# Kernel optimization log

Hardware: AMD Instinct MI355X
Metric: run time of the kernel (lower is better)

## Reference

```python
import jax, jax.numpy as jnp
import numpy as np

H = 64  # hidden_dimension
F = 8   # number_of_input_features
P = 64  # prediction_length
B = 1024
T = 512


def _lstm_cell(x, h, c, Wih, Whh, bih, bhh):
    # PyTorch gate order: input, forget, cell(g), output
    gates = x @ Wih.T + h @ Whh.T + (bih + bhh)  # [B, 4H]
    i, f, g, o = jnp.split(gates, 4, axis=-1)
    c_new = jax.nn.sigmoid(f) * c + jax.nn.sigmoid(i) * jnp.tanh(g)
    h_new = jax.nn.sigmoid(o) * jnp.tanh(c_new)
    return h_new, c_new


def setup_inputs() -> dict:
    key = jax.random.key(0)
    ks = jax.random.split(key, 11)
    s = 1.0 / np.sqrt(H)
    u = lambda k, shape: jax.random.uniform(k, shape, jnp.float32, -s, s)
    return {
        "input_sequence": jax.random.normal(ks[0], (B, T, F), jnp.float32),
        "enc_Wih": u(ks[1], (4 * H, F)),
        "enc_Whh": u(ks[2], (4 * H, H)),
        "enc_bih": u(ks[3], (4 * H,)),
        "enc_bhh": u(ks[4], (4 * H,)),
        "dec_Wih": u(ks[5], (4 * H, F)),
        "dec_Whh": u(ks[6], (4 * H, H)),
        "dec_bih": u(ks[7], (4 * H,)),
        "dec_bhh": u(ks[8], (4 * H,)),
        "fc_W": u(ks[9], (F, H)),
        "fc_b": u(ks[10], (F,)),
    }


def reference(input_sequence, enc_Wih, enc_Whh, enc_bih, enc_bhh,
              dec_Wih, dec_Whh, dec_bih, dec_bhh, fc_W, fc_b):
    Bn = input_sequence.shape[0]
    h0 = jnp.zeros((Bn, H), input_sequence.dtype)
    c0 = jnp.zeros((Bn, H), input_sequence.dtype)

    # ---- Encoder: scan over time ----
    xs = jnp.swapaxes(input_sequence, 0, 1)  # [T, B, F]

    def enc_step(carry, x_t):
        h, c = carry
        h, c = _lstm_cell(x_t, h, c, enc_Wih, enc_Whh, enc_bih, enc_bhh)
        return (h, c), None

    (h, c), _ = jax.lax.scan(enc_step, (h0, c0), xs)

    x_last = input_sequence[:, -1, :]  # [B, F]

    def dec_step(carry, _):
        h, c, x = carry
        h, c = _lstm_cell(x, h, c, dec_Wih, dec_Whh, dec_bih, dec_bhh)
        pred = h @ fc_W.T + fc_b  # [B, F]
        return (h, c, pred), pred

    _, preds = jax.lax.scan(dec_step, (h, c, x_last), None, length=P)
    return jnp.swapaxes(preds, 0, 1)  # [B, P, F]
```

## Files before the change

### kernel.cpp

```cpp
#include <hip/hip_runtime.h>


#define Hh 64
#define Ff 8
#define Tt 512
#define Pp 64
#define BATCH 1024
#define MB 4
#define NBLK (BATCH / MB)
#define ROWS 72
#define ABUF (16 * ROWS + 64)
#define XSTRIDE 32

typedef __attribute__((ext_vector_type(8))) _Float16 half8;
typedef __attribute__((ext_vector_type(4))) _Float16 half4;
typedef __attribute__((ext_vector_type(4))) float f32x4;

#define LOG2E  1.44269504088896340736f
#define K2LOG2 2.88538008177792681472f

#define MFMA16(a, b, c) __builtin_amdgcn_mfma_f32_16x16x32_f16(a, b, c, 0, 0, 0)

__device__ __forceinline__ float rcp_(float x)  { return __builtin_amdgcn_rcpf(x); }
__device__ __forceinline__ float exp2_(float x) { return __builtin_amdgcn_exp2f(x); }
__device__ __forceinline__ int arow_base(int m) { return m * ROWS + (m & 3) * 16; }

__device__ __forceinline__ void load_wfrags(
    const float* __restrict__ Whh, const float* __restrict__ Wih,
    int wv, int q, int col, half8 w0[4], half8 w1[4], half8 wx[4])
{
    #pragma unroll
    for (int Tg = 0; Tg < 4; ++Tg) {
        int g = Tg * 64 + wv * 16 + col;
        float sc = (Tg == 2) ? K2LOG2 : LOG2E;
        const float* r0 = Whh + g * 64 + q * 8;
        #pragma unroll
        for (int j = 0; j < 8; ++j) {
            w0[Tg][j] = (_Float16)(r0[j] * sc);
            w1[Tg][j] = (_Float16)(r0[32 + j] * sc);
            wx[Tg][j] = (q == 0) ? (_Float16)(Wih[g * 8 + j] * sc) : (_Float16)0.f;
        }
    }
}

__device__ __forceinline__ void pchain(half8 ax, const half8 wx[4],
                                       const f32x4 biasv[4], f32x4 P[4])
{
    P[2] = MFMA16(ax, wx[2], biasv[2]);
    P[0] = MFMA16(ax, wx[0], biasv[0]);
    P[1] = MFMA16(ax, wx[1], biasv[1]);
    P[3] = MFMA16(ax, wx[3], biasv[3]);
}

__device__ __forceinline__ void qgates(half8 a0, half8 a1,
    const half8 w0[4], const half8 w1[4], const f32x4 P[4], f32x4 Q[4])
{
    Q[2] = MFMA16(a0, w0[2], P[2]);
    Q[2] = MFMA16(a1, w1[2], Q[2]);
    Q[0] = MFMA16(a0, w0[0], P[0]);
    Q[0] = MFMA16(a1, w1[0], Q[0]);
    Q[1] = MFMA16(a0, w0[1], P[1]);
    Q[1] = MFMA16(a1, w1[1], Q[1]);
    Q[3] = MFMA16(a0, w0[3], P[3]);
    Q[3] = MFMA16(a1, w1[3], Q[3]);
}

__device__ __forceinline__ float cellf(const f32x4 Q[4], float& cS)
{
    float eg = exp2_(Q[2][0]);
    float ei = exp2_(-Q[0][0]);
    float it = (eg - 1.f) * rcp_((1.f + ei) * (1.f + eg));
    float ef = exp2_(-Q[1][0]);
    float sf = rcp_(1.f + ef);
    float eo = exp2_(-Q[3][0]);
    float so   = rcp_(1.f + eo);
    float m2so = -2.f * so;
    cS = __builtin_fmaf(sf, cS, K2LOG2 * it);
    float cc = __builtin_amdgcn_fmed3f(cS, -60.f, 60.f);
    float ec = exp2_(cc);
    float rc = rcp_(1.f + ec);
    return __builtin_fmaf(m2so, rc, so);
}

__global__ __launch_bounds__(256, 1)
void seq2seq_v16(const float* __restrict__ x_seq,
                 const float* __restrict__ eWih, const float* __restrict__ eWhh,
                 const float* __restrict__ ebih, const float* __restrict__ ebhh,
                 const float* __restrict__ dWih, const float* __restrict__ dWhh,
                 const float* __restrict__ dbih, const float* __restrict__ dbhh,
                 const float* __restrict__ fcW,  const float* __restrict__ fcb,
                 float* __restrict__ out)
{
    __shared__ __align__(16) _Float16 xs[(Tt + 2) * XSTRIDE];
    __shared__ __align__(16) _Float16 A0[ABUF];
    __shared__ __align__(16) _Float16 A1[ABUF];

    const int tid  = threadIdx.x;
    const int wv   = tid >> 6;
    const int lane = tid & 63;
    const int q    = lane >> 4;
    const int col  = lane & 15;
    const int u    = wv * 16 + col;
    const int b0   = blockIdx.x * MB;

    half8 w0[4], w1[4], wx[4];
    load_wfrags(eWhh, eWih, wv, q, col, w0, w1, wx);
    f32x4 biasv[4];
    #pragma unroll
    for (int Tg = 0; Tg < 4; ++Tg) {
        int g = Tg * 64 + u;
        float sc = (Tg == 2) ? K2LOG2 : LOG2E;
        float bv = (ebih[g] + ebhh[g]) * sc;
        biasv[Tg] = (f32x4){bv, bv, bv, bv};
    }

    { int* Z0 = (int*)A0; int* Z1 = (int*)A1;
      for (int i = tid; i < ABUF / 2; i += 256) { Z0[i] = 0; Z1[i] = 0; } }
    if (tid < 32) ((int*)xs)[Tt * 16 + tid] = 0;
    for (int i = tid; i < MB * Tt * 2; i += 256) {
        int b   = i >> 10;
        int rem = i & 1023;
        int t   = rem >> 1;
        int f4  = (rem & 1) * 4;
        const float* src = x_seq + ((size_t)(b0 + b) * Tt + t) * Ff + f4;
        half4 s = { (_Float16)src[0], (_Float16)src[1], (_Float16)src[2], (_Float16)src[3] };
        *(half4*)(&xs[t * XSTRIDE + b * 8 + f4]) = s;
    }
    __syncthreads();

    const _Float16* arA = A0 + arow_base(col) + q * 8;
    const _Float16* arB = A1 + arow_base(col) + q * 8;
    _Float16* hwA = A0 + 4 * q * ROWS + u;
    _Float16* hwB = A1 + 4 * q * ROWS + u;
    const _Float16* xq = xs + (col >> 2) * 8;

    float cS = 0.f;
    f32x4 P[4];
    {   half8 ax = *(const half8*)(xq);
        pchain(ax, wx, biasv, P);
        xq += XSTRIDE; }

    for (int t = 0; t < Tt; t += 2) {
        __syncthreads();
        {
            half8 a0 = *(const half8*)(arA);
            half8 a1 = *(const half8*)(arA + 32);
            half8 ax = *(const half8*)(xq); xq += XSTRIDE;
            f32x4 Q[4];
            qgates(a0, a1, w0, w1, P, Q);
            pchain(ax, wx, biasv, P);
            float hn = cellf(Q, cS);
            *hwB = (_Float16)hn;
        }
        __syncthreads();
        {
            half8 a0 = *(const half8*)(arB);
            half8 a1 = *(const half8*)(arB + 32);
            half8 ax = *(const half8*)(xq); xq += XSTRIDE;
            f32x4 Q[4];
            qgates(a0, a1, w0, w1, P, Q);
            pchain(ax, wx, biasv, P);
            float hn = cellf(Q, cS);
            *hwA = (_Float16)hn;
        }
    }

    half8 axl = *(const half8*)(xs + (Tt - 1) * XSTRIDE + (col >> 2) * 8);

    half8 wp0[4], wp1[4];
    f32x4 biasp[4];
    #pragma unroll
    for (int Tg = 0; Tg < 4; ++Tg) {
        int g = Tg * 64 + u;
        float sc = (Tg == 2) ? K2LOG2 : LOG2E;
        #pragma unroll
        for (int j = 0; j < 8; ++j) {
            int k0 = q * 8 + j;
            float v0 = dWhh[g * 64 + k0];
            float v1 = dWhh[g * 64 + 32 + k0];
            w0[Tg][j] = (_Float16)(v0 * sc);
            w1[Tg][j] = (_Float16)(v1 * sc);
            wx[Tg][j] = (q == 0) ? (_Float16)(dWih[g * 8 + j] * sc) : (_Float16)0.f;
            float s0 = v0, s1 = v1;
            #pragma unroll
            for (int f = 0; f < 8; ++f) {
                float wif = dWih[g * 8 + f];
                s0 = __builtin_fmaf(wif, fcW[f * 64 + k0], s0);
                s1 = __builtin_fmaf(wif, fcW[f * 64 + 32 + k0], s1);
            }
            wp0[Tg][j] = (_Float16)(s0 * sc);
            wp1[Tg][j] = (_Float16)(s1 * sc);
        }
        float bb = dbih[g] + dbhh[g];
        float bp = bb;
        #pragma unroll
        for (int f = 0; f < 8; ++f) bp = __builtin_fmaf(dWih[g * 8 + f], fcb[f], bp);
        biasv[Tg] = (f32x4){bb * sc, bb * sc, bb * sc, bb * sc};
        biasp[Tg] = (f32x4){bp * sc, bp * sc, bp * sc, bp * sc};
    }
    half8 wf0, wf1;
    f32x4 biasf;
    {
        #pragma unroll
        for (int j = 0; j < 8; ++j) {
            wf0[j] = (col < 8) ? (_Float16)fcW[col * 64 + q * 8 + j]      : (_Float16)0.f;
            wf1[j] = (col < 8) ? (_Float16)fcW[col * 64 + 32 + q * 8 + j] : (_Float16)0.f;
        }
        float fb = (col < 8) ? fcb[col] : 0.f;
        biasf = (f32x4){fb, fb, fb, fb};
    }

    float* predbuf = (float*)xs;
    const bool pw = (wv == 0) && (col < 8);

    pchain(axl, wx, biasv, P);
    __syncthreads();
    {
        half8 a0 = *(const half8*)(arA);
        half8 a1 = *(const half8*)(arA + 32);
        f32x4 Q[4];
        qgates(a0, a1, w0, w1, P, Q);
        float hn = cellf(Q, cS);
        *hwB = (_Float16)hn;
    }

    for (int p = 1; p < Pp; ++p) {
        __syncthreads();
        const _Float16* ar = (p & 1) ? arB : arA;
        _Float16*       hw = (p & 1) ? hwA : hwB;
        half8 a0 = *(const half8*)(ar);
        half8 a1 = *(const half8*)(ar + 32);
        f32x4 Q[4];
        qgates(a0, a1, wp0, wp1, biasp, Q);
        f32x4 F = MFMA16(a0, wf0, biasf);
        F       = MFMA16(a1, wf1, F);
        float hn = cellf(Q, cS);
        *hw = (_Float16)hn;
        if (pw) predbuf[q * (Pp * Ff) + (p - 1) * Ff + col] = F[0];
    }

    __syncthreads();
    {
        half8 a0 = *(const half8*)(arA);
        half8 a1 = *(const half8*)(arA + 32);
        f32x4 F = MFMA16(a0, wf0, biasf);
        F       = MFMA16(a1, wf1, F);
        if (pw) predbuf[q * (Pp * Ff) + (Pp - 1) * Ff + col] = F[0];
    }
    __syncthreads();

    {
        f32x4* out4 = (f32x4*)out + (size_t)b0 * (Pp * Ff / 4);
        const f32x4* pb4 = (const f32x4*)predbuf;
        for (int i = tid; i < MB * Pp * Ff / 4; i += 256)
            out4[i] = pb4[i];
    }
}

extern "C" void kernel_launch(void* const* d_in, const int* in_sizes, int n_in,
                              void* d_out, int out_size, void* d_ws, size_t ws_size,
                              hipStream_t stream) {
    (void)in_sizes; (void)n_in; (void)d_ws; (void)ws_size; (void)out_size;
    hipLaunchKernelGGL(seq2seq_v16, dim3(NBLK), dim3(256), 0, stream,
                       (const float*)d_in[0],
                       (const float*)d_in[1], (const float*)d_in[2],
                       (const float*)d_in[3], (const float*)d_in[4],
                       (const float*)d_in[5], (const float*)d_in[6],
                       (const float*)d_in[7], (const float*)d_in[8],
                       (const float*)d_in[9], (const float*)d_in[10],
                       (float*)d_out);
}
```

Before: 218.4 us.

## Compute input projection with one MFMA per step via lane-selected operand

```diff
diff --git a/kernel.cpp b/kernel.cpp
--- a/kernel.cpp
+++ b/kernel.cpp
@@ -26,8 +26,8 @@
 __device__ __forceinline__ int arow_base(int m) { return m * ROWS + (m & 3) * 16; }
 
 __device__ __forceinline__ void load_wfrags(
-    const float* __restrict__ Whh, const float* __restrict__ Wih,
-    int wv, int q, int col, half8 w0[4], half8 w1[4], half8 wx[4])
+    const float* __restrict__ Whh, int wv, int q, int col,
+    half8 w0[4], half8 w1[4])
 {
     #pragma unroll
     for (int Tg = 0; Tg < 4; ++Tg) {
@@ -38,31 +38,38 @@
         for (int j = 0; j < 8; ++j) {
             w0[Tg][j] = (_Float16)(r0[j] * sc);
             w1[Tg][j] = (_Float16)(r0[32 + j] * sc);
-            wx[Tg][j] = (q == 0) ? (_Float16)(Wih[g * 8 + j] * sc) : (_Float16)0.f;
-        }
-    }
-}
-
-__device__ __forceinline__ void pchain(half8 ax, const half8 wx[4],
-                                       const f32x4 biasv[4], f32x4 P[4])
-{
-    P[2] = MFMA16(ax, wx[2], biasv[2]);
-    P[0] = MFMA16(ax, wx[0], biasv[0]);
-    P[1] = MFMA16(ax, wx[1], biasv[1]);
-    P[3] = MFMA16(ax, wx[3], biasv[3]);
+        }
+    }
 }
 
 __device__ __forceinline__ void qgates(half8 a0, half8 a1,
-    const half8 w0[4], const half8 w1[4], const f32x4 P[4], f32x4 Q[4])
-{
-    Q[2] = MFMA16(a0, w0[2], P[2]);
+    const half8 w0[4], const half8 w1[4], const f32x4 Ci[4], f32x4 Q[4])
+{
+    Q[2] = MFMA16(a0, w0[2], Ci[2]);
     Q[2] = MFMA16(a1, w1[2], Q[2]);
-    Q[0] = MFMA16(a0, w0[0], P[0]);
+    Q[0] = MFMA16(a0, w0[0], Ci[0]);
     Q[0] = MFMA16(a1, w1[0], Q[0]);
-    Q[1] = MFMA16(a0, w0[1], P[1]);
+    Q[1] = MFMA16(a0, w0[1], Ci[1]);
     Q[1] = MFMA16(a1, w1[1], Q[1]);
-    Q[3] = MFMA16(a0, w0[3], P[3]);
+    Q[3] = MFMA16(a0, w0[3], Ci[3]);
     Q[3] = MFMA16(a1, w1[3], Q[3]);
+}
+
+__device__ __forceinline__ float cellf3(const f32x4 Q[4], f32x4 P4, float& cS)
+{
+    float eg = exp2_(Q[2][0] + P4[2]);
+    float ei = exp2_(-(Q[0][0] + P4[0]));
+    float it = (eg - 1.f) * rcp_((1.f + ei) * (1.f + eg));
+    float ef = exp2_(-(Q[1][0] + P4[1]));
+    float sf = rcp_(1.f + ef);
+    float eo = exp2_(-(Q[3][0] + P4[3]));
+    float so   = rcp_(1.f + eo);
+    float m2so = -2.f * so;
+    cS = __builtin_fmaf(sf, cS, K2LOG2 * it);
+    float cc = __builtin_amdgcn_fmed3f(cS, -60.f, 60.f);
+    float ec = exp2_(cc);
+    float rc = rcp_(1.f + ec);
+    return __builtin_fmaf(m2so, rc, so);
 }
 
 __device__ __forceinline__ float cellf(const f32x4 Q[4], float& cS)
@@ -83,7 +90,7 @@
 }
 
 __global__ __launch_bounds__(256, 1)
-void seq2seq_v16(const float* __restrict__ x_seq,
+void seq2seq_v18(const float* __restrict__ x_seq,
                  const float* __restrict__ eWih, const float* __restrict__ eWhh,
                  const float* __restrict__ ebih, const float* __restrict__ ebhh,
                  const float* __restrict__ dWih, const float* __restrict__ dWhh,
@@ -102,9 +109,12 @@
     const int col  = lane & 15;
     const int u    = wv * 16 + col;
     const int b0   = blockIdx.x * MB;
-
-    half8 w0[4], w1[4], wx[4];
-    load_wfrags(eWhh, eWih, wv, q, col, w0, w1, wx);
+    const bool selq = (q == (col & 3));
+    const half8 hz = {};
+    const f32x4 Zv = {0.f, 0.f, 0.f, 0.f};
+
+    half8 w0[4], w1[4];
+    load_wfrags(eWhh, wv, q, col, w0, w1);
     f32x4 biasv[4];
     #pragma unroll
     for (int Tg = 0; Tg < 4; ++Tg) {
@@ -113,6 +123,10 @@
         float bv = (ebih[g] + ebhh[g]) * sc;
         biasv[Tg] = (f32x4){bv, bv, bv, bv};
     }
+    half8 Bx;
+    #pragma unroll
+    for (int j = 0; j < 8; ++j)
+        Bx[j] = (_Float16)(eWih[(q * 64 + u) * 8 + j] * ((q == 2) ? K2LOG2 : LOG2E));
 
     { int* Z0 = (int*)A0; int* Z1 = (int*)A1;
       for (int i = tid; i < ABUF / 2; i += 256) { Z0[i] = 0; Z1[i] = 0; } }
@@ -135,32 +149,33 @@
     const _Float16* xq = xs + (col >> 2) * 8;
 
     float cS = 0.f;
-    f32x4 P[4];
-    {   half8 ax = *(const half8*)(xq);
-        pchain(ax, wx, biasv, P);
-        xq += XSTRIDE; }
+    f32x4 P4a, P4b;
+    half8 xvA, xvB;
+    {   half8 xv0 = *(const half8*)(xq); xq += XSTRIDE;
+        xvA        = *(const half8*)(xq); xq += XSTRIDE;
+        P4a = MFMA16(selq ? xv0 : hz, Bx, Zv); }
 
     for (int t = 0; t < Tt; t += 2) {
         __syncthreads();
         {
             half8 a0 = *(const half8*)(arA);
             half8 a1 = *(const half8*)(arA + 32);
-            half8 ax = *(const half8*)(xq); xq += XSTRIDE;
+            P4b = MFMA16(selq ? xvA : hz, Bx, Zv);
+            xvB = *(const half8*)(xq); xq += XSTRIDE;
             f32x4 Q[4];
-            qgates(a0, a1, w0, w1, P, Q);
-            pchain(ax, wx, biasv, P);
-            float hn = cellf(Q, cS);
+            qgates(a0, a1, w0, w1, biasv, Q);
+            float hn = cellf3(Q, P4a, cS);
             *hwB = (_Float16)hn;
         }
         __syncthreads();
         {
             half8 a0 = *(const half8*)(arB);
             half8 a1 = *(const half8*)(arB + 32);
-            half8 ax = *(const half8*)(xq); xq += XSTRIDE;
+            P4a = MFMA16(selq ? xvB : hz, Bx, Zv);
+            xvA = *(const half8*)(xq); xq += XSTRIDE;
             f32x4 Q[4];
-            qgates(a0, a1, w0, w1, P, Q);
-            pchain(ax, wx, biasv, P);
-            float hn = cellf(Q, cS);
+            qgates(a0, a1, w0, w1, biasv, Q);
+            float hn = cellf3(Q, P4b, cS);
             *hwA = (_Float16)hn;
         }
     }
@@ -180,7 +195,6 @@
             float v1 = dWhh[g * 64 + 32 + k0];
             w0[Tg][j] = (_Float16)(v0 * sc);
             w1[Tg][j] = (_Float16)(v1 * sc);
-            wx[Tg][j] = (q == 0) ? (_Float16)(dWih[g * 8 + j] * sc) : (_Float16)0.f;
             float s0 = v0, s1 = v1;
             #pragma unroll
             for (int f = 0; f < 8; ++f) {
@@ -198,6 +212,9 @@
         biasv[Tg] = (f32x4){bb * sc, bb * sc, bb * sc, bb * sc};
         biasp[Tg] = (f32x4){bp * sc, bp * sc, bp * sc, bp * sc};
     }
+    #pragma unroll
+    for (int j = 0; j < 8; ++j)
+        Bx[j] = (_Float16)(dWih[(q * 64 + u) * 8 + j] * ((q == 2) ? K2LOG2 : LOG2E));
     half8 wf0, wf1;
     f32x4 biasf;
     {
@@ -213,14 +230,14 @@
     float* predbuf = (float*)xs;
     const bool pw = (wv == 0) && (col < 8);
 
-    pchain(axl, wx, biasv, P);
+    P4a = MFMA16(selq ? axl : hz, Bx, Zv);
     __syncthreads();
     {
         half8 a0 = *(const half8*)(arA);
         half8 a1 = *(const half8*)(arA + 32);
         f32x4 Q[4];
-        qgates(a0, a1, w0, w1, P, Q);
-        float hn = cellf(Q, cS);
+        qgates(a0, a1, w0, w1, biasv, Q);
+        float hn = cellf3(Q, P4a, cS);
         *hwB = (_Float16)hn;
     }
 
@@ -232,10 +249,10 @@
         half8 a1 = *(const half8*)(ar + 32);
         f32x4 Q[4];
         qgates(a0, a1, wp0, wp1, biasp, Q);
+        float hn = cellf(Q, cS);
+        *hw = (_Float16)hn;
         f32x4 F = MFMA16(a0, wf0, biasf);
         F       = MFMA16(a1, wf1, F);
-        float hn = cellf(Q, cS);
-        *hw = (_Float16)hn;
         if (pw) predbuf[q * (Pp * Ff) + (p - 1) * Ff + col] = F[0];
     }
 
@@ -261,7 +278,7 @@
                               void* d_out, int out_size, void* d_ws, size_t ws_size,
                               hipStream_t stream) {
     (void)in_sizes; (void)n_in; (void)d_ws; (void)ws_size; (void)out_size;
-    hipLaunchKernelGGL(seq2seq_v16, dim3(NBLK), dim3(256), 0, stream,
+    hipLaunchKernelGGL(seq2seq_v18, dim3(NBLK), dim3(256), 0, stream,
                        (const float*)d_in[0],
                        (const float*)d_in[1], (const float*)d_in[2],
                        (const float*)d_in[3], (const float*)d_in[4],
```

Measured after the change: 225.7 us. 1.03x slower.
